# Kernel optimization log

Hardware: AMD Instinct MI355X
Metric: run time of the kernel (lower is better)

The kernel has to match this reference:

```python
import jax, jax.numpy as jnp
import numpy as np

N = 3_000_000  # batch of deformation gradients


def setup_inputs() -> dict:
    key = jax.random.key(0)
    eye = jnp.eye(3, dtype=jnp.float32)
    noise = jax.random.normal(key, (N, 3, 3), dtype=jnp.float32)
    # near-identity deformation gradients so det(F) > 0 (log J well-defined)
    F = eye[None, :, :] + 0.05 * noise
    return {"F": F}


def _energy(F):
    """Strain energy density W(F) per sample. F: [N,3,3]."""
    g = jnp.array([4.0, 0.5, 0.5], dtype=F.dtype)  # transversely isotropic structural tensor (diagonal)
    C = jnp.einsum('nji,njk->nik', F, F)           # right Cauchy-Green C = F^T F, [N,3,3]
    I1 = jnp.trace(C, axis1=1, axis2=2)            # tr(C)
    J = jnp.linalg.det(F)                          # det(F)
    cofC = (J ** 2)[:, None, None] * jnp.linalg.inv(C)  # cof(C) = det(C) C^{-1}, det(C) = J^2
    I4 = jnp.einsum('nii,i->n', C, g)              # tr(C G), G diagonal
    I5 = jnp.einsum('nii,i->n', cofC, g)           # tr(cof(C) G)
    return 8.0 * I1 + 10.0 * J ** 2 - 56.0 * jnp.log(J) + 0.2 * (I4 ** 2 + I5 ** 2) - 44.0


def reference(F):
    # P = dW/dF, computed per sample; grad of the batch-sum gives per-sample grads
    return jax.grad(lambda f: jnp.sum(_energy(f)))(F)
```

## Files before the change

### kernel.cpp

```cpp
#include <hip/hip_runtime.h>


typedef float f2 __attribute__((ext_vector_type(2)));

#define SAMPLES_PER_BLOCK 512
#define F2_PER_BLOCK (SAMPLES_PER_BLOCK * 9 / 2)

__global__ __launch_bounds__(256) void pk1_grad_kernel(
    const f2* __restrict__ Fin, f2* __restrict__ Pout, int total2)
{
    __shared__ f2 lds2[F2_PER_BLOCK];
    const int t = threadIdx.x;
    const int base2 = blockIdx.x * F2_PER_BLOCK;

#pragma unroll
    for (int j = 0; j < 9; ++j) {
        int i = j * 256 + t;
        int g = base2 + i;
        f2 v;
        if (g < total2) v = Fin[g];
        else { v.x = 1.0f; v.y = 1.0f; }
        lds2[i] = v;
    }
    __syncthreads();

    float buf[18];
#pragma unroll
    for (int q = 0; q < 9; ++q) {
        f2 v = lds2[t * 9 + q];
        buf[2 * q]     = v.x;
        buf[2 * q + 1] = v.y;
    }

#pragma unroll
    for (int s = 0; s < 2; ++s) {
        float f[9];
#pragma unroll
        for (int k = 0; k < 9; ++k) f[k] = buf[s * 9 + k];

        float c00 = f[4]*f[8] - f[5]*f[7];
        float c01 = f[5]*f[6] - f[3]*f[8];
        float c02 = f[3]*f[7] - f[4]*f[6];
        float c10 = f[2]*f[7] - f[1]*f[8];
        float c11 = f[0]*f[8] - f[2]*f[6];
        float c12 = f[1]*f[6] - f[0]*f[7];
        float c20 = f[1]*f[5] - f[2]*f[4];
        float c21 = f[2]*f[3] - f[0]*f[5];
        float c22 = f[0]*f[4] - f[1]*f[3];
        float J    = f[0]*c00 + f[1]*c01 + f[2]*c02;
        float invJ = 1.0f / J;

        float C00 = f[0]*f[0] + f[3]*f[3] + f[6]*f[6];
        float C11 = f[1]*f[1] + f[4]*f[4] + f[7]*f[7];
        float C22 = f[2]*f[2] + f[5]*f[5] + f[8]*f[8];
        float C01 = f[0]*f[1] + f[3]*f[4] + f[6]*f[7];
        float C02 = f[0]*f[2] + f[3]*f[5] + f[6]*f[8];
        float C12 = f[1]*f[2] + f[4]*f[5] + f[7]*f[8];

        float I4 = 4.0f*C00 + 0.5f*(C11 + C22);

        float K00 = C11*C22 - C12*C12;
        float K11 = C00*C22 - C02*C02;
        float K22 = C00*C11 - C01*C01;
        float K01 = C02*C12 - C01*C22;
        float K02 = C01*C12 - C02*C11;
        float K12 = C01*C02 - C00*C12;

        float I5 = 4.0f*K00 + 0.5f*(K11 + K22);

        float J2    = J * J;
        float alpha = (20.0f*J2 - 56.0f + 0.8f*I5*I5) * invJ;
        float beta  = 0.8f * I4;
        float gamma = -0.8f * I5 * invJ;

        float cf[3][3] = {{c00,c01,c02},{c10,c11,c12},{c20,c21,c22}};
        float K[3][3]  = {{K00,K01,K02},{K01,K11,K12},{K02,K12,K22}};
        const float gv[3] = {4.0f, 0.5f, 0.5f};

#pragma unroll
        for (int i = 0; i < 3; ++i) {
            float a0 = cf[i][0] * 4.0f;
            float a1 = cf[i][1] * 0.5f;
            float a2 = cf[i][2] * 0.5f;
#pragma unroll
            for (int j = 0; j < 3; ++j) {
                float M = a0 * K[0][j] + a1 * K[1][j] + a2 * K[2][j];
                buf[s * 9 + 3 * i + j] =
                      (16.0f + beta * gv[j]) * f[3 * i + j]
                    + alpha * cf[i][j]
                    + gamma * M;
            }
        }
    }

#pragma unroll
    for (int q = 0; q < 9; ++q) {
        f2 v;
        v.x = buf[2 * q];
        v.y = buf[2 * q + 1];
        lds2[t * 9 + q] = v;
    }
    __syncthreads();

#pragma unroll
    for (int j = 0; j < 9; ++j) {
        int i = j * 256 + t;
        int g = base2 + i;
        if (g < total2) Pout[g] = lds2[i];
    }
}

extern "C" void kernel_launch(void* const* d_in, const int* in_sizes, int n_in,
                              void* d_out, int out_size, void* d_ws, size_t ws_size,
                              hipStream_t stream) {
    const f2* F = (const f2*)d_in[0];
    f2* P = (f2*)d_out;
    int total2 = in_sizes[0] / 2;
    int blocks = (total2 + F2_PER_BLOCK - 1) / F2_PER_BLOCK;
    pk1_grad_kernel<<<blocks, 256, 0, stream>>>(F, P, total2);
}
```

Before: 39.74 us.

## Use persistent blocks with register prefetch of the next tile

The one-block-per-tile launch becomes a fixed grid of 1024 persistent blocks that loop over tiles. Each block prefetches the next tile's inputs into registers while computing the current one, and separate LDS buffers are used for input and output staging. The aim is to overlap global loads with compute and to cut block launch overhead. In exchange it raises register pressure and relies on a fixed grid size that may underfill or unbalance the GPU.

```diff
diff --git a/kernel.cpp b/kernel.cpp
--- a/kernel.cpp
+++ b/kernel.cpp
@@ -3,110 +3,130 @@
 
 typedef float f2 __attribute__((ext_vector_type(2)));
 
-#define SAMPLES_PER_BLOCK 512
-#define F2_PER_BLOCK (SAMPLES_PER_BLOCK * 9 / 2)
+#define TPB 256
+#define SAMPLES_PER_TILE 512
+#define F2_PER_TILE (SAMPLES_PER_TILE * 9 / 2)
+#define NBLOCKS 1024
 
-__global__ __launch_bounds__(256) void pk1_grad_kernel(
-    const f2* __restrict__ Fin, f2* __restrict__ Pout, int total2)
+__global__ __launch_bounds__(TPB) void pk1_grad_kernel(
+    const f2* __restrict__ Fin, f2* __restrict__ Pout, int total2, int ntiles)
 {
-    __shared__ f2 lds2[F2_PER_BLOCK];
+    __shared__ f2 ldsX[F2_PER_TILE];
+    __shared__ f2 ldsY[F2_PER_TILE];
     const int t = threadIdx.x;
-    const int base2 = blockIdx.x * F2_PER_BLOCK;
 
+    f2 pre[9];
+    {
+        const int base2 = blockIdx.x * F2_PER_TILE;
 #pragma unroll
-    for (int j = 0; j < 9; ++j) {
-        int i = j * 256 + t;
-        int g = base2 + i;
-        f2 v;
-        if (g < total2) v = Fin[g];
-        else { v.x = 1.0f; v.y = 1.0f; }
-        lds2[i] = v;
-    }
-    __syncthreads();
-
-    float buf[18];
-#pragma unroll
-    for (int q = 0; q < 9; ++q) {
-        f2 v = lds2[t * 9 + q];
-        buf[2 * q]     = v.x;
-        buf[2 * q + 1] = v.y;
-    }
-
-#pragma unroll
-    for (int s = 0; s < 2; ++s) {
-        float f[9];
-#pragma unroll
-        for (int k = 0; k < 9; ++k) f[k] = buf[s * 9 + k];
-
-        float c00 = f[4]*f[8] - f[5]*f[7];
-        float c01 = f[5]*f[6] - f[3]*f[8];
-        float c02 = f[3]*f[7] - f[4]*f[6];
-        float c10 = f[2]*f[7] - f[1]*f[8];
-        float c11 = f[0]*f[8] - f[2]*f[6];
-        float c12 = f[1]*f[6] - f[0]*f[7];
-        float c20 = f[1]*f[5] - f[2]*f[4];
-        float c21 = f[2]*f[3] - f[0]*f[5];
-        float c22 = f[0]*f[4] - f[1]*f[3];
-        float J    = f[0]*c00 + f[1]*c01 + f[2]*c02;
-        float invJ = 1.0f / J;
-
-        float C00 = f[0]*f[0] + f[3]*f[3] + f[6]*f[6];
-        float C11 = f[1]*f[1] + f[4]*f[4] + f[7]*f[7];
-        float C22 = f[2]*f[2] + f[5]*f[5] + f[8]*f[8];
-        float C01 = f[0]*f[1] + f[3]*f[4] + f[6]*f[7];
-        float C02 = f[0]*f[2] + f[3]*f[5] + f[6]*f[8];
-        float C12 = f[1]*f[2] + f[4]*f[5] + f[7]*f[8];
-
-        float I4 = 4.0f*C00 + 0.5f*(C11 + C22);
-
-        float K00 = C11*C22 - C12*C12;
-        float K11 = C00*C22 - C02*C02;
-        float K22 = C00*C11 - C01*C01;
-        float K01 = C02*C12 - C01*C22;
-        float K02 = C01*C12 - C02*C11;
-        float K12 = C01*C02 - C00*C12;
-
-        float I5 = 4.0f*K00 + 0.5f*(K11 + K22);
-
-        float J2    = J * J;
-        float alpha = (20.0f*J2 - 56.0f + 0.8f*I5*I5) * invJ;
-        float beta  = 0.8f * I4;
-        float gamma = -0.8f * I5 * invJ;
-
-        float cf[3][3] = {{c00,c01,c02},{c10,c11,c12},{c20,c21,c22}};
-        float K[3][3]  = {{K00,K01,K02},{K01,K11,K12},{K02,K12,K22}};
-        const float gv[3] = {4.0f, 0.5f, 0.5f};
-
-#pragma unroll
-        for (int i = 0; i < 3; ++i) {
-            float a0 = cf[i][0] * 4.0f;
-            float a1 = cf[i][1] * 0.5f;
-            float a2 = cf[i][2] * 0.5f;
-#pragma unroll
-            for (int j = 0; j < 3; ++j) {
-                float M = a0 * K[0][j] + a1 * K[1][j] + a2 * K[2][j];
-                buf[s * 9 + 3 * i + j] =
-                      (16.0f + beta * gv[j]) * f[3 * i + j]
-                    + alpha * cf[i][j]
-                    + gamma * M;
-            }
+        for (int q = 0; q < 9; ++q) {
+            int g = base2 + q * TPB + t;
+            if (g < total2) pre[q] = Fin[g];
+            else { pre[q].x = 1.0f; pre[q].y = 1.0f; }
         }
     }
 
-#pragma unroll
-    for (int q = 0; q < 9; ++q) {
-        f2 v;
-        v.x = buf[2 * q];
-        v.y = buf[2 * q + 1];
-        lds2[t * 9 + q] = v;
-    }
-    __syncthreads();
+    for (int tile = blockIdx.x; tile < ntiles; tile += NBLOCKS) {
+        const int base2 = tile * F2_PER_TILE;
 
 #pragma unroll
-    for (int j = 0; j < 9; ++j) {
-        int i = j * 256 + t;
-        int g = base2 + i;
-        if (g < total2) Pout[g] = lds2[i];
+        for (int q = 0; q < 9; ++q) ldsX[q * TPB + t] = pre[q];
+        __syncthreads();
+
+        const int ntile = tile + NBLOCKS;
+        if (ntile < ntiles) {
+            const int nbase2 = ntile * F2_PER_TILE;
+#pragma unroll
+            for (int q = 0; q < 9; ++q) {
+                int g = nbase2 + q * TPB + t;
+                if (g < total2) pre[q] = Fin[g];
+                else { pre[q].x = 1.0f; pre[q].y = 1.0f; }
+            }
+        }
+
+        float buf[18];
+#pragma unroll
+        for (int q = 0; q < 9; ++q) {
+            f2 v = ldsX[t * 9 + q];
+            buf[2 * q]     = v.x;
+            buf[2 * q + 1] = v.y;
+        }
+
+#pragma unroll
+        for (int s = 0; s < 2; ++s) {
+            float f[9];
+#pragma unroll
+            for (int k = 0; k < 9; ++k) f[k] = buf[s * 9 + k];
+
+            float c00 = f[4]*f[8] - f[5]*f[7];
+            float c01 = f[5]*f[6] - f[3]*f[8];
+            float c02 = f[3]*f[7] - f[4]*f[6];
+            float c10 = f[2]*f[7] - f[1]*f[8];
+            float c11 = f[0]*f[8] - f[2]*f[6];
+            float c12 = f[1]*f[6] - f[0]*f[7];
+            float c20 = f[1]*f[5] - f[2]*f[4];
+            float c21 = f[2]*f[3] - f[0]*f[5];
+            float c22 = f[0]*f[4] - f[1]*f[3];
+            float J    = f[0]*c00 + f[1]*c01 + f[2]*c02;
+            float invJ = 1.0f / J;
+
+            float C00 = f[0]*f[0] + f[3]*f[3] + f[6]*f[6];
+            float C11 = f[1]*f[1] + f[4]*f[4] + f[7]*f[7];
+            float C22 = f[2]*f[2] + f[5]*f[5] + f[8]*f[8];
+            float C01 = f[0]*f[1] + f[3]*f[4] + f[6]*f[7];
+            float C02 = f[0]*f[2] + f[3]*f[5] + f[6]*f[8];
+            float C12 = f[1]*f[2] + f[4]*f[5] + f[7]*f[8];
+
+            float I4 = 4.0f*C00 + 0.5f*(C11 + C22);
+
+            float K00 = C11*C22 - C12*C12;
+            float K11 = C00*C22 - C02*C02;
+            float K22 = C00*C11 - C01*C01;
+            float K01 = C02*C12 - C01*C22;
+            float K02 = C01*C12 - C02*C11;
+            float K12 = C01*C02 - C00*C12;
+
+            float I5 = 4.0f*K00 + 0.5f*(K11 + K22);
+
+            float J2    = J * J;
+            float alpha = (20.0f*J2 - 56.0f + 0.8f*I5*I5) * invJ;
+            float beta  = 0.8f * I4;
+            float gamma = -0.8f * I5 * invJ;
+
+            float cf[3][3] = {{c00,c01,c02},{c10,c11,c12},{c20,c21,c22}};
+            float K[3][3]  = {{K00,K01,K02},{K01,K11,K12},{K02,K12,K22}};
+            const float gv[3] = {4.0f, 0.5f, 0.5f};
+
+#pragma unroll
+            for (int i = 0; i < 3; ++i) {
+                float a0 = cf[i][0] * 4.0f;
+                float a1 = cf[i][1] * 0.5f;
+                float a2 = cf[i][2] * 0.5f;
+#pragma unroll
+                for (int j = 0; j < 3; ++j) {
+                    float M = a0 * K[0][j] + a1 * K[1][j] + a2 * K[2][j];
+                    buf[s * 9 + 3 * i + j] =
+                          (16.0f + beta * gv[j]) * f[3 * i + j]
+                        + alpha * cf[i][j]
+                        + gamma * M;
+                }
+            }
+        }
+
+#pragma unroll
+        for (int q = 0; q < 9; ++q) {
+            f2 v;
+            v.x = buf[2 * q];
+            v.y = buf[2 * q + 1];
+            ldsY[t * 9 + q] = v;
+        }
+        __syncthreads();
+
+#pragma unroll
+        for (int q = 0; q < 9; ++q) {
+            int g = base2 + q * TPB + t;
+            if (g < total2) Pout[g] = ldsY[q * TPB + t];
+        }
     }
 }
 
@@ -116,6 +136,6 @@
     const f2* F = (const f2*)d_in[0];
     f2* P = (f2*)d_out;
     int total2 = in_sizes[0] / 2;
-    int blocks = (total2 + F2_PER_BLOCK - 1) / F2_PER_BLOCK;
-    pk1_grad_kernel<<<blocks, 256, 0, stream>>>(F, P, total2);
+    int ntiles = (total2 + F2_PER_TILE - 1) / F2_PER_TILE;
+    pk1_grad_kernel<<<NBLOCKS, TPB, 0, stream>>>(F, P, total2, ntiles);
 }
```

After: 38.68 us. -2.7%, faster.
